# Optimization experiments

Hardware: AMD Instinct MI355X
Metric: run time of the kernel (lower is better)

## Reference

```python
import jax, jax.numpy as jnp
import numpy as np

PAD_IDX = 0        # assumed padding index (not defined in source snippet)
LAMBDA = 1.0       # lambda_bias buffer value
B, S, D, H = 2, 2048, 1024, 16
HD = D // H        # head_dim = 64
SCALE = HD ** -0.5


def setup_inputs() -> dict:
    key = jax.random.key(0)
    ks = jax.random.split(key, 18)
    w = lambda k: jax.random.normal(k, (D, D), jnp.float32) * 0.02
    b = lambda k: jax.random.normal(k, (D,), jnp.float32) * 0.02
    return {
        "query": jax.random.normal(ks[0], (B, S, D), jnp.float32),
        "key":   jax.random.normal(ks[1], (B, S, D), jnp.float32),
        "value": jax.random.normal(ks[2], (B, S, D), jnp.float32),
        # minval=1 for field_ids so no token is PAD -> no all--inf softmax rows
        "field_ids":      jax.random.randint(ks[3], (B, S), 1, 32),
        "entity_ids":     jax.random.randint(ks[4], (B, S), 0, 64),
        "time_ids":       jax.random.randint(ks[5], (B, S), 0, 128),
        "token_type_ids": jax.random.randint(ks[6], (B, S), 0, 8),
        "edge_ids":       jax.random.randint(ks[7], (B, S), 0, 4),
        "role_ids":       jax.random.randint(ks[8], (B, S), 0, 8),
        "Wq": w(ks[9]),  "bq": b(ks[10]),
        "Wk": w(ks[11]), "bk": b(ks[12]),
        "Wv": w(ks[13]), "bv": b(ks[14]),
        "Wo": w(ks[15]), "bo": b(ks[16]),
    }


def _bias_matrix(field_ids, entity_ids, time_ids, token_type_ids, edge_ids, role_ids):
    # pairwise equality bias, shape [B, S, S]
    eq = lambda x: (x[:, :, None] == x[:, None, :]).astype(jnp.float32)
    has_edge = ((edge_ids[:, :, None] != PAD_IDX) | (edge_ids[:, None, :] != PAD_IDX)).astype(jnp.float32)
    bias = (eq(field_ids)
            + eq(entity_ids)
            + 0.5 * eq(time_ids)
            + 0.3 * eq(token_type_ids)
            + 1.5 * has_edge
            + 0.5 * eq(role_ids))
    is_pad = field_ids == PAD_IDX
    pad_mask = is_pad[:, :, None] | is_pad[:, None, :]
    return jnp.where(pad_mask, -jnp.inf, bias)


def reference(query, key, value, field_ids, entity_ids, time_ids, token_type_ids,
              edge_ids, role_ids, Wq, bq, Wk, bk, Wv, bv, Wo, bo):
    Bsz, Sq, _ = query.shape
    Q = (query @ Wq.T + bq).reshape(Bsz, Sq, H, HD)
    K = (key   @ Wk.T + bk).reshape(Bsz, Sq, H, HD)
    V = (value @ Wv.T + bv).reshape(Bsz, Sq, H, HD)
    # [B, H, S, S]
    scores = jnp.einsum('bihd,bjhd->bhij', Q, K) * SCALE
    B_struct = _bias_matrix(field_ids, entity_ids, time_ids, token_type_ids, edge_ids, role_ids)
    scores = scores + LAMBDA * B_struct[:, None, :, :]
    attn = jax.nn.softmax(scores, axis=-1)
    out = jnp.einsum('bhij,bjhd->bihd', attn, V).reshape(Bsz, Sq, D)
    return out @ Wo.T + bo
```

## Files before the change

### kernel.cpp

```cpp
#include <hip/hip_runtime.h>
#include <hip/hip_bf16.h>
#include <stdint.h>

#define B_N 2
#define S_N 2048
#define D_N 1024
#define H_N 16
#define LOG2E 1.44269504f

using bf8    = __attribute__((ext_vector_type(8))) short;
using us8    = __attribute__((ext_vector_type(8))) unsigned short;
using f32x4  = __attribute__((ext_vector_type(4))) float;
using f32x16 = __attribute__((ext_vector_type(16))) float;

static __device__ __forceinline__ ushort f2b(float f) {
  uint32_t u = __builtin_bit_cast(uint32_t, f);
  u += 0x7fffu + ((u >> 16) & 1u);
  return (ushort)(u >> 16);
}

static __device__ __forceinline__ uint32_t cvtpk(float a, float b) {
  uint32_t r;
  asm("v_cvt_pk_bf16_f32 %0, %1, %2" : "=v"(r) : "v"(a), "v"(b));
  return r;
}

static __device__ __forceinline__ float h2f(ushort u) {
  return (float)__builtin_bit_cast(_Float16, u);
}

static __device__ __forceinline__ ushort h16(float x) {
  return __builtin_bit_cast(ushort, (_Float16)x);
}

typedef __attribute__((address_space(1))) const uint32_t GU32;
typedef __attribute__((address_space(3))) uint32_t LU32;
static __device__ __forceinline__ void gload16(const void* g, void* l) {
  __builtin_amdgcn_global_load_lds((GU32*)g, (LU32*)l, 16, 0, 0);
}

static __device__ __forceinline__ void cvt4B(const float* __restrict__ s, ushort* __restrict__ d, int i) {
  float4 v = *(const float4*)(s + i);
  ushort4 o;
  o.x = f2b(v.x); o.y = f2b(v.y); o.z = f2b(v.z); o.w = f2b(v.w);
  *(ushort4*)(d + i) = o;
}

__global__ __launch_bounds__(256) void prep_kernel(
    const float* __restrict__ q, const float* __restrict__ k, const float* __restrict__ v,
    const float* __restrict__ wq, const float* __restrict__ wk, const float* __restrict__ wv,
    const float* __restrict__ wo,
    ushort* __restrict__ oq, ushort* __restrict__ ok, ushort* __restrict__ ov,
    ushort* __restrict__ owq, ushort* __restrict__ owk, ushort* __restrict__ owv,
    ushort* __restrict__ owo,
    const int* __restrict__ f, const int* __restrict__ e, const int* __restrict__ ti,
    const int* __restrict__ tt, const int* __restrict__ ed, const int* __restrict__ ro,
    uint32_t* __restrict__ codes) {
  int x = blockIdx.x;
  if (x < 12288) {
    int which = x >> 12, i = (x & 4095) * 1024 + threadIdx.x * 4;
    const float* s = (which == 0) ? q : (which == 1) ? k : v;
    ushort* d = (which == 0) ? oq : (which == 1) ? ok : ov;
    cvt4B(s, d, i);
  } else if (x < 16384) {
    int which = (x - 12288) >> 10, i = (x & 1023) * 1024 + threadIdx.x * 4;
    const float* s = (which == 0) ? wq : (which == 1) ? wk : (which == 2) ? wv : wo;
    ushort* d = (which == 0) ? owq : (which == 1) ? owk : (which == 2) ? owv : owo;
    cvt4B(s, d, i);
  } else {
    int i = (x - 16384) * 256 + threadIdx.x;
    uint32_t c = ((uint32_t)f[i] & 31u) | (((uint32_t)e[i] & 63u) << 5) |
                 (((uint32_t)ti[i] & 127u) << 11) | (((uint32_t)tt[i] & 7u) << 18) |
                 (((uint32_t)ro[i] & 7u) << 21) |
                 ((ed[i] != 0) ? (1u << 24) : 0u) | ((f[i] == 0) ? (1u << 25) : 0u);
    codes[i] = c;
  }
}

static __device__ __forceinline__ float bias_val(uint32_t a, uint32_t b) {
  uint32_t x = a ^ b;
  uint32_t o = a | b;
  float v = (o & 0x1000000u) ? 1.5f : 0.0f;
  v += (x & 0x1Fu)     ? 0.0f : 1.0f;
  v += (x & 0x7E0u)    ? 0.0f : 1.0f;
  v += (x & 0x3F800u)  ? 0.0f : 0.5f;
  v += (x & 0x1C0000u) ? 0.0f : 0.3f;
  v += (x & 0xE00000u) ? 0.0f : 0.5f;
  return (o & 0x2000000u) ? -30000.f : v;
}

__global__ __launch_bounds__(256) void bias_build(const uint32_t* __restrict__ codes,
                                                  ushort* __restrict__ BF) {
  int t = blockIdx.x * 256 + threadIdx.x;
  int v8    = t & 1;
  int lane  = (t >> 1) & 63;
  int h     = (t >> 7) & 1;
  int kvt   = (t >> 8) & 31;
  int qtile = (t >> 13) & 63;
  int b     = t >> 19;
  int hi = lane >> 5;
  int q  = qtile * 32 + (lane & 31);
  uint32_t cq = codes[b * S_N + q];
  int kvb = kvt * 64 + h * 32 + v8 * 16 + hi * 4;
  uint4 c0 = *(const uint4*)(codes + b * S_N + kvb);
  uint4 c1 = *(const uint4*)(codes + b * S_N + kvb + 8);
  ushort o[8];
  o[0] = h16(bias_val(cq, c0.x) * LOG2E);
  o[1] = h16(bias_val(cq, c0.y) * LOG2E);
  o[2] = h16(bias_val(cq, c0.z) * LOG2E);
  o[3] = h16(bias_val(cq, c0.w) * LOG2E);
  o[4] = h16(bias_val(cq, c1.x) * LOG2E);
  o[5] = h16(bias_val(cq, c1.y) * LOG2E);
  o[6] = h16(bias_val(cq, c1.z) * LOG2E);
  o[7] = h16(bias_val(cq, c1.w) * LOG2E);
  *(uint4*)(BF + (size_t)t * 8) = *(const uint4*)o;
}

template <int MODE>
static __device__ __forceinline__ void gemm_core(ushort* As, ushort* Bs,
    const ushort* __restrict__ A, const ushort* __restrict__ W, const float* __restrict__ bias,
    void* __restrict__ out, float scale) {
  const int tid = threadIdx.x, lane = tid & 63, wid = tid >> 6;
  const int g = lane >> 4, c = lane & 15;
  const int wm = wid >> 1, wn = wid & 1;
  const int m0 = blockIdx.y * 128, n0 = blockIdx.x * 128;

  f32x4 acc[4][4];
#pragma unroll
  for (int i = 0; i < 4; ++i)
#pragma unroll
    for (int j = 0; j < 4; ++j) acc[i][j] = (f32x4){0.f, 0.f, 0.f, 0.f};

  for (int k0 = 0; k0 < D_N; k0 += 32) {
#pragma unroll
    for (int j = 0; j < 2; ++j) {
      int idx = tid + j * 256;
      int row = idx >> 2, c8 = (idx & 3) * 8;
      gload16(A + (size_t)(m0 + row) * D_N + k0 + c8, As + idx * 8);
      gload16(W + (size_t)(n0 + row) * D_N + k0 + c8, Bs + idx * 8);
    }
    __syncthreads();
    bf8 af[4], bw[4];
#pragma unroll
    for (int mi = 0; mi < 4; ++mi) af[mi] = *(const bf8*)(As + (wm * 64 + mi * 16 + c) * 32 + g * 8);
#pragma unroll
    for (int ni = 0; ni < 4; ++ni) bw[ni] = *(const bf8*)(Bs + (wn * 64 + ni * 16 + c) * 32 + g * 8);
#pragma unroll
    for (int mi = 0; mi < 4; ++mi)
#pragma unroll
      for (int ni = 0; ni < 4; ++ni)
        acc[mi][ni] = __builtin_amdgcn_mfma_f32_16x16x32_bf16(af[mi], bw[ni], acc[mi][ni], 0, 0, 0);
    __syncthreads();
  }

#pragma unroll
  for (int mi = 0; mi < 4; ++mi)
#pragma unroll
    for (int ni = 0; ni < 4; ++ni) {
      int ncol = n0 + wn * 64 + ni * 16 + c;
      float bv = bias[ncol];
      int hh = ncol >> 6, dd = ncol & 63;
      if (MODE == 2) {
        int mb = m0 + wm * 64 + mi * 16 + g * 4;
        int bb = mb >> 11, kv = mb & 2047;
        int kvt = kv >> 6, kin = kv & 63;
        int ks = kin >> 4, hif = (kin >> 3) & 1, e = kin & 7;
        int jj = dd >> 5, l31v = dd & 31;
        int lanef = hif * 32 + l31v;
        size_t off = (((size_t)(bb * H_N + hh) * 32 + kvt) * 8 + ks * 2 + jj) * 512 + lanef * 8 + e;
        ushort4 o4;
        o4.x = f2b((acc[mi][ni][0] + bv) * scale);
        o4.y = f2b((acc[mi][ni][1] + bv) * scale);
        o4.z = f2b((acc[mi][ni][2] + bv) * scale);
        o4.w = f2b((acc[mi][ni][3] + bv) * scale);
        *(ushort4*)((ushort*)out + off) = o4;
      } else {
#pragma unroll
        for (int r = 0; r < 4; ++r) {
          int m = m0 + wm * 64 + mi * 16 + g * 4 + r;
          float v = (acc[mi][ni][r] + bv) * scale;
          if (MODE == 0) {
            int bb = m >> 11, q = m & 2047;
            int qtile = q >> 5, l31q = q & 31;
            int ks = dd >> 4, hif = (dd >> 3) & 1, e = dd & 7;
            int lanef = hif * 32 + l31q;
            size_t off = (((size_t)(bb * H_N + hh) * 64 + qtile) * 4 + ks) * 512 + lanef * 8 + e;
            ((ushort*)out)[off] = f2b(v);
          } else if (MODE == 3) {
            int bb = m >> 11, s = m & 2047;
            int kvt = s >> 6, sin = s & 63;
            int jj = sin >> 5, l31k = sin & 31;
            int ks = dd >> 4, hif = (dd >> 3) & 1, e = dd & 7;
            int lanef = hif * 32 + l31k;
            size_t off = (((size_t)(bb * H_N + hh) * 32 + kvt) * 8 + ks * 2 + jj) * 512 + lanef * 8 + e;
            ((ushort*)out)[off] = f2b(v);
          } else {
            ((float*)out)[(size_t)m * D_N + ncol] = v;
          }
        }
      }
    }
}

__global__ __launch_bounds__(256) void gemm_qkv(
    const ushort* __restrict__ Xq, const ushort* __restrict__ Xk, const ushort* __restrict__ Xv,
    const ushort* __restrict__ Wq, const ushort* __restrict__ Wk, const ushort* __restrict__ Wv,
    const float* __restrict__ bq, const float* __restrict__ bk, const float* __restrict__ bv,
    ushort* __restrict__ Qo, ushort* __restrict__ Ko, ushort* __restrict__ Vo) {
  __shared__ __align__(16) ushort As[128 * 32];
  __shared__ __align__(16) ushort Bs[128 * 32];
  if (blockIdx.z == 0)      gemm_core<0>(As, Bs, Xq, Wq, bq, Qo, 0.125f * LOG2E);
  else if (blockIdx.z == 1) gemm_core<3>(As, Bs, Xk, Wk, bk, Ko, 1.0f);
  else                      gemm_core<2>(As, Bs, Xv, Wv, bv, Vo, 1.0f);
}

__global__ __launch_bounds__(256) void gemm_o(const ushort* __restrict__ A, const ushort* __restrict__ W,
                                              const float* __restrict__ bias, float* __restrict__ out) {
  __shared__ __align__(16) ushort As[128 * 32];
  __shared__ __align__(16) ushort Bs[128 * 32];
  gemm_core<1>(As, Bs, A, W, bias, out, 1.0f);
}

__global__ __launch_bounds__(256, 2) void attn_kernel(const ushort* __restrict__ QF, const ushort* __restrict__ KF,
                                                      const ushort* __restrict__ VF, const ushort* __restrict__ BF,
                                                      ushort* __restrict__ AO) {
  const int tid = threadIdx.x, lane = tid & 63, w = tid >> 6;
  const int l31 = lane & 31, hi = lane >> 5;
  const int raw = blockIdx.x;
  const int bh = (raw & 7) * 4 + ((raw >> 3) & 3);
  const int x  = raw >> 5;
  const int b = bh >> 4, h = bh & 15;
  const int qtile = x * 4 + w;

  const ushort* Qp = QF + ((size_t)(bh * 64 + qtile) * 4) * 512 + lane * 8;
  bf8 aq[4];
#pragma unroll
  for (int ks = 0; ks < 4; ++ks) aq[ks] = *(const bf8*)(Qp + ks * 512);

  const ushort* Ku = KF + (size_t)bh * 32 * 8 * 512;
  const ushort* Vu = VF + (size_t)bh * 32 * 8 * 512;
  const ushort* Bu = BF + (size_t)(b * 64 + qtile) * 32 * 2048;
  const int koff = lane * 8;
  const int boff = lane * 16;

  float lr = 0.f;
  f32x16 o0, o1;
#pragma unroll
  for (int r = 0; r < 16; ++r) { o0[r] = 0.f; o1[r] = 0.f; }

  const int CROW0[16] = {0,1,2,3, 8,9,10,11, 16,17,18,19, 24,25,26,27};

  auto LOADK = [&](bf8 (&kf)[4][2], int t) {
    const ushort* p = Ku + (size_t)t * 4096 + koff;
#pragma unroll
    for (int ks = 0; ks < 4; ++ks) {
      kf[ks][0] = *(const bf8*)(p + (ks * 2 + 0) * 512);
      kf[ks][1] = *(const bf8*)(p + (ks * 2 + 1) * 512);
    }
  };
  auto LOADV = [&](bf8 (&vf)[4][2], int t) {
    const ushort* p = Vu + (size_t)t * 4096 + koff;
#pragma unroll
    for (int ks = 0; ks < 4; ++ks) {
      vf[ks][0] = *(const bf8*)(p + (ks * 2 + 0) * 512);
      vf[ks][1] = *(const bf8*)(p + (ks * 2 + 1) * 512);
    }
  };
  auto LOADB = [&](us8 (&bb)[4], int t) {
    const ushort* p = Bu + (size_t)t * 2048 + boff;
    bb[0] = *(const us8*)(p);
    bb[1] = *(const us8*)(p + 8);
    bb[2] = *(const us8*)(p + 1024);
    bb[3] = *(const us8*)(p + 1024 + 8);
  };

  auto TILE = [&](const bf8 (&kf)[4][2], const bf8 (&vf)[4][2], const us8 (&bb)[4]) {
    f32x16 s0, s1;
#pragma unroll
    for (int g = 0; g < 4; ++g)
#pragma unroll
      for (int j = 0; j < 4; ++j) {
        s0[g * 4 + j] = h2f(bb[g >> 1][(g & 1) * 4 + j]);
        s1[g * 4 + j] = h2f(bb[2 + (g >> 1)][(g & 1) * 4 + j]);
      }
    __builtin_amdgcn_s_setprio(1);
#pragma unroll
    for (int ks = 0; ks < 4; ++ks) {
      s0 = __builtin_amdgcn_mfma_f32_32x32x16_bf16(kf[ks][0], aq[ks], s0, 0, 0, 0);
      s1 = __builtin_amdgcn_mfma_f32_32x32x16_bf16(kf[ks][1], aq[ks], s1, 0, 0, 0);
    }
    __builtin_amdgcn_s_setprio(0);

#pragma unroll
    for (int r = 0; r < 16; ++r) {
      s0[r] = __builtin_exp2f(s0[r]);
      s1[r] = __builtin_exp2f(s1[r]);
    }
    float a8[8];
#pragma unroll
    for (int r = 0; r < 8; ++r)
      a8[r] = (s0[r] + s0[r + 8]) + (s1[r] + s1[r + 8]);
    lr += ((a8[0] + a8[4]) + (a8[1] + a8[5])) + ((a8[2] + a8[6]) + (a8[3] + a8[7]));

    bf8 pa[4];
#pragma unroll
    for (int t = 0; t < 2; ++t) {
      uint32_t wv[4][2];
#pragma unroll
      for (int g = 0; g < 4; ++g) {
        const float* sp = (t == 0) ? (const float*)&s0 : (const float*)&s1;
        wv[g][0] = cvtpk(sp[g * 4 + 0], sp[g * 4 + 1]);
        wv[g][1] = cvtpk(sp[g * 4 + 2], sp[g * 4 + 3]);
      }
#pragma unroll
      for (int pr = 0; pr < 2; ++pr) {
        uint32_t x0 = hi ? wv[2 * pr][0] : wv[2 * pr + 1][0];
        uint32_t x1 = hi ? wv[2 * pr][1] : wv[2 * pr + 1][1];
        uint32_t r0 = (uint32_t)__shfl_xor((int)x0, 32);
        uint32_t r1 = (uint32_t)__shfl_xor((int)x1, 32);
        uint4 pw;
        pw.x = hi ? r0 : wv[2 * pr][0];
        pw.y = hi ? r1 : wv[2 * pr][1];
        pw.z = hi ? wv[2 * pr + 1][0] : r0;
        pw.w = hi ? wv[2 * pr + 1][1] : r1;
        pa[t * 2 + pr] = __builtin_bit_cast(bf8, pw);
      }
    }

    __builtin_amdgcn_s_setprio(1);
#pragma unroll
    for (int ks = 0; ks < 4; ++ks) {
      o0 = __builtin_amdgcn_mfma_f32_32x32x16_bf16(pa[ks], vf[ks][0], o0, 0, 0, 0);
      o1 = __builtin_amdgcn_mfma_f32_32x32x16_bf16(pa[ks], vf[ks][1], o1, 0, 0, 0);
    }
    __builtin_amdgcn_s_setprio(0);
  };

  bf8 kA[4][2], kB[4][2], vA[4][2], vB[4][2];
  us8 bA[4], bB[4];
  LOADK(kA, 0); LOADB(bA, 0); LOADV(vA, 0);

#pragma unroll 1
  for (int p = 0; p < 15; ++p) {
    int t = 2 * p;
    LOADK(kB, t + 1); LOADB(bB, t + 1); LOADV(vB, t + 1);
    TILE(kA, vA, bA);
    LOADK(kA, t + 2); LOADB(bA, t + 2); LOADV(vA, t + 2);
    TILE(kB, vB, bB);
  }
  LOADK(kB, 31); LOADB(bB, 31); LOADV(vB, 31);
  TILE(kA, vA, bA);
  TILE(kB, vB, bB);

  lr += __shfl_xor(lr, 32);
  float inv = 1.0f / lr;
#pragma unroll
  for (int r = 0; r < 16; ++r) {
    float ivr = __shfl(inv, CROW0[r] + 4 * hi);
    int q = qtile * 32 + CROW0[r] + 4 * hi;
    size_t base = ((size_t)b * S_N + q) * D_N + h * 64 + l31;
    AO[base]      = f2b(o0[r] * ivr);
    AO[base + 32] = f2b(o1[r] * ivr);
  }
}

extern "C" void kernel_launch(void* const* d_in, const int* in_sizes, int n_in,
                              void* d_out, int out_size, void* d_ws, size_t ws_size,
                              hipStream_t stream) {
  (void)in_sizes; (void)n_in; (void)out_size; (void)ws_size;
  const float* query = (const float*)d_in[0];
  const float* key_  = (const float*)d_in[1];
  const float* value = (const float*)d_in[2];
  const int* fid  = (const int*)d_in[3];
  const int* eid  = (const int*)d_in[4];
  const int* tmid = (const int*)d_in[5];
  const int* ttid = (const int*)d_in[6];
  const int* edid = (const int*)d_in[7];
  const int* rlid = (const int*)d_in[8];
  const float* Wq = (const float*)d_in[9];  const float* bq = (const float*)d_in[10];
  const float* Wk = (const float*)d_in[11]; const float* bk = (const float*)d_in[12];
  const float* Wv = (const float*)d_in[13]; const float* bv = (const float*)d_in[14];
  const float* Wo = (const float*)d_in[15]; const float* bo = (const float*)d_in[16];

  char* ws = (char*)d_ws;
  const size_t MB = 1024 * 1024;
  ushort* Xq  = (ushort*)(ws);
  ushort* Xk  = (ushort*)(ws + 8 * MB);
  ushort* Xv  = (ushort*)(ws + 16 * MB);
  ushort* Wqb = (ushort*)(ws + 24 * MB);
  ushort* Wkb = (ushort*)(ws + 26 * MB);
  ushort* Wvb = (ushort*)(ws + 28 * MB);
  ushort* BF  = (ushort*)(ws);
  ushort* QFw = (ushort*)(ws + 30 * MB);
  ushort* KFw = (ushort*)(ws + 38 * MB);
  ushort* VFw = (ushort*)(ws + 46 * MB);
  ushort* AOw = (ushort*)(ws + 54 * MB);
  ushort* Wob = (ushort*)(ws + 62 * MB);
  uint32_t* codes = (uint32_t*)(ws + 64 * MB);

  prep_kernel<<<16400, 256, 0, stream>>>(query, key_, value, Wq, Wk, Wv, Wo,
                                         Xq, Xk, Xv, Wqb, Wkb, Wvb, Wob,
                                         fid, eid, tmid, ttid, edid, rlid, codes);
  gemm_qkv<<<dim3(D_N / 128, (B_N * S_N) / 128, 3), 256, 0, stream>>>(
      Xq, Xk, Xv, Wqb, Wkb, Wvb, bq, bk, bv, QFw, KFw, VFw);
  bias_build<<<4096, 256, 0, stream>>>(codes, BF);
  attn_kernel<<<512, 256, 0, stream>>>(QFw, KFw, VFw, BF, AOw);
  gemm_o<<<dim3(D_N / 128, (B_N * S_N) / 128), 256, 0, stream>>>(AOw, Wob, bo, (float*)d_out);
}
```

Measured before the change: 157.5 us.

## Give output projection its own 64x128 tile GEMM and relax attention launch bounds

Replaces the shared gemm_core path for the output projection with a dedicated kernel using 64-row by 128-column tiles, doubling the grid to 512 blocks so more CUs stay busy for this 4096x1024x1024 GEMM. Each wave computes a 64x32 slab with 16x16x32 bf16 MFMAs and writes fp32 output plus bias directly. The now-unused fp32 store branch is removed from gemm_core. It also changes the attention kernel launch bound from 2 to 1 blocks per CU minimum, giving the compiler more registers at the risk of lower occupancy. The new GEMM keeps a single-buffered load/sync loop with no prefetch, so load latency stays exposed.

```diff
diff --git a/kernel.cpp b/kernel.cpp
--- a/kernel.cpp
+++ b/kernel.cpp
@@ -186,7 +186,7 @@
             int lanef = hif * 32 + l31q;
             size_t off = (((size_t)(bb * H_N + hh) * 64 + qtile) * 4 + ks) * 512 + lanef * 8 + e;
             ((ushort*)out)[off] = f2b(v);
-          } else if (MODE == 3) {
+          } else {
             int bb = m >> 11, s = m & 2047;
             int kvt = s >> 6, sin = s & 63;
             int jj = sin >> 5, l31k = sin & 31;
@@ -194,8 +194,6 @@
             int lanef = hif * 32 + l31k;
             size_t off = (((size_t)(bb * H_N + hh) * 32 + kvt) * 8 + ks * 2 + jj) * 512 + lanef * 8 + e;
             ((ushort*)out)[off] = f2b(v);
-          } else {
-            ((float*)out)[(size_t)m * D_N + ncol] = v;
           }
         }
       }
@@ -216,12 +214,58 @@
 
 __global__ __launch_bounds__(256) void gemm_o(const ushort* __restrict__ A, const ushort* __restrict__ W,
                                               const float* __restrict__ bias, float* __restrict__ out) {
-  __shared__ __align__(16) ushort As[128 * 32];
+  __shared__ __align__(16) ushort As[64 * 32];
   __shared__ __align__(16) ushort Bs[128 * 32];
-  gemm_core<1>(As, Bs, A, W, bias, out, 1.0f);
-}
-
-__global__ __launch_bounds__(256, 2) void attn_kernel(const ushort* __restrict__ QF, const ushort* __restrict__ KF,
+  const int tid = threadIdx.x, lane = tid & 63, wn = tid >> 6;
+  const int g = lane >> 4, c = lane & 15;
+  const int m0 = blockIdx.y * 64, n0 = blockIdx.x * 128;
+
+  f32x4 acc[4][2];
+#pragma unroll
+  for (int i = 0; i < 4; ++i)
+#pragma unroll
+    for (int j = 0; j < 2; ++j) acc[i][j] = (f32x4){0.f, 0.f, 0.f, 0.f};
+
+  for (int k0 = 0; k0 < D_N; k0 += 32) {
+    {
+      int row = tid >> 2, c8 = (tid & 3) * 8;
+      gload16(A + (size_t)(m0 + row) * D_N + k0 + c8, As + tid * 8);
+    }
+#pragma unroll
+    for (int j = 0; j < 2; ++j) {
+      int idx = tid + j * 256;
+      int row = idx >> 2, c8 = (idx & 3) * 8;
+      gload16(W + (size_t)(n0 + row) * D_N + k0 + c8, Bs + idx * 8);
+    }
+    __syncthreads();
+    bf8 af[4], bw[2];
+#pragma unroll
+    for (int mi = 0; mi < 4; ++mi) af[mi] = *(const bf8*)(As + (mi * 16 + c) * 32 + g * 8);
+#pragma unroll
+    for (int ni = 0; ni < 2; ++ni) bw[ni] = *(const bf8*)(Bs + (wn * 32 + ni * 16 + c) * 32 + g * 8);
+#pragma unroll
+    for (int mi = 0; mi < 4; ++mi)
+#pragma unroll
+      for (int ni = 0; ni < 2; ++ni)
+        acc[mi][ni] = __builtin_amdgcn_mfma_f32_16x16x32_bf16(af[mi], bw[ni], acc[mi][ni], 0, 0, 0);
+    __syncthreads();
+  }
+
+#pragma unroll
+  for (int mi = 0; mi < 4; ++mi)
+#pragma unroll
+    for (int ni = 0; ni < 2; ++ni) {
+      int ncol = n0 + wn * 32 + ni * 16 + c;
+      float bv = bias[ncol];
+#pragma unroll
+      for (int r = 0; r < 4; ++r) {
+        int m = m0 + mi * 16 + g * 4 + r;
+        out[(size_t)m * D_N + ncol] = acc[mi][ni][r] + bv;
+      }
+    }
+}
+
+__global__ __launch_bounds__(256, 1) void attn_kernel(const ushort* __restrict__ QF, const ushort* __restrict__ KF,
                                                       const ushort* __restrict__ VF, const ushort* __restrict__ BF,
                                                       ushort* __restrict__ AO) {
   const int tid = threadIdx.x, lane = tid & 63, w = tid >> 6;
@@ -405,5 +449,5 @@
       Xq, Xk, Xv, Wqb, Wkb, Wvb, bq, bk, bv, QFw, KFw, VFw);
   bias_build<<<4096, 256, 0, stream>>>(codes, BF);
   attn_kernel<<<512, 256, 0, stream>>>(QFw, KFw, VFw, BF, AOw);
-  gemm_o<<<dim3(D_N / 128, (B_N * S_N) / 128), 256, 0, stream>>>(AOw, Wob, bo, (float*)d_out);
-}
+  gemm_o<<<dim3(D_N / 128, (B_N * S_N) / 64), 256, 0, stream>>>(AOw, Wob, bo, (float*)d_out);
+}
```

Measured after the change: 172.3 us. 1.09x slower.
